# Kernel tuning notes

Measured on AMD Instinct MI355X. Metric: run time of the kernel, lower is better.

Reference implementation:

```python
import jax, jax.numpy as jnp
import numpy as np

K = 16  # neighbors per node (dgl.knn_graph k)


def _knn_indices(centers, k):
    # pairwise squared distances [N, N]
    sq = jnp.sum(centers * centers, axis=1)
    d2 = sq[:, None] + sq[None, :] - 2.0 * (centers @ centers.T)
    # k nearest (includes self at distance ~0), edges: neighbor(src) -> node(dst)
    _, idx = jax.lax.top_k(-d2, k)  # [N, k]
    return idx


def _graph_conv(h, idx, src_norm, dst_norm, W, b):
    # DGL GraphConv, norm='both': D_out^{-1/2} A D_in^{-1/2} H W + b
    hs = h * src_norm[:, None]          # scale by out-degree^{-1/2}
    agg = jnp.sum(hs[idx], axis=1)      # sum over k neighbors -> [N, F]
    agg = agg * dst_norm                # in-degree is exactly k for knn graph
    return agg @ W + b


def setup_inputs() -> dict:
    key = jax.random.key(0)
    ks = jax.random.split(key, 8)
    N, D, H = 20000, 128, 256
    s_in, s_h = 1.0 / np.sqrt(D), 1.0 / np.sqrt(H)
    return {
        "x": jax.random.normal(ks[0], (N, D), dtype=jnp.float32),
        "centers": jax.random.normal(ks[1], (N, 3), dtype=jnp.float32),
        "W0": jax.random.normal(ks[2], (D, H), dtype=jnp.float32) * s_in,
        "b0": jnp.zeros((H,), dtype=jnp.float32),
        "W1": jax.random.normal(ks[3], (H, H), dtype=jnp.float32) * s_h,
        "b1": jnp.zeros((H,), dtype=jnp.float32),
        "W2": jax.random.normal(ks[4], (H, H), dtype=jnp.float32) * s_h,
        "b2": jnp.zeros((H,), dtype=jnp.float32),
        "Wf": jax.random.normal(ks[5], (H, 1), dtype=jnp.float32) * s_h,
        "bf": jnp.zeros((1,), dtype=jnp.float32),
    }


def reference(x, centers, W0, b0, W1, b1, W2, b2, Wf, bf):
    N = x.shape[0]
    idx = _knn_indices(centers, K)  # [N, K] src nodes per dst node
    # out-degree of each node = number of times it appears as a neighbor
    out_deg = jnp.zeros((N,), dtype=x.dtype).at[idx.reshape(-1)].add(1.0)
    src_norm = jax.lax.rsqrt(jnp.maximum(out_deg, 1.0))
    dst_norm = 1.0 / jnp.sqrt(jnp.asarray(K, dtype=x.dtype))  # in-degree == K
    h = x
    for W, b in ((W0, b0), (W1, b1), (W2, b2)):
        h = jax.nn.relu(_graph_conv(h, idx, src_norm, dst_norm, W, b))
    logits = (h @ Wf + bf).squeeze(-1)  # [N]
    return jax.nn.sigmoid(logits)
```

## Files before the change

### kernel.cpp

```cpp
#include <hip/hip_runtime.h>
#include <math.h>

#define KNN 16
#define G 32
#define G3 32768
#define MRING 31
#define FLTMAX 3.402823466e+38f

typedef __attribute__((ext_vector_type(8))) short short8x;
typedef __attribute__((ext_vector_type(4))) float f32x4;

__device__ __forceinline__ unsigned short bf16rn(float x) {
  unsigned u = __float_as_uint(x);
  unsigned r = (u + 0x7FFFu + ((u >> 16) & 1u)) >> 16;
  return (unsigned short)r;
}
__device__ __forceinline__ float bf16tof(unsigned short h) {
  return __uint_as_float(((unsigned)h) << 16);
}

__device__ __forceinline__ unsigned fkey(float f) {
  unsigned u = __float_as_uint(f);
  return (u & 0x80000000u) ? ~u : (u | 0x80000000u);
}
__device__ __forceinline__ float funkey(unsigned u) {
  unsigned b = (u & 0x80000000u) ? (u & 0x7FFFFFFFu) : ~u;
  return __uint_as_float(b);
}

__device__ __forceinline__ void cell_of(float x, float y, float z, const float* P,
                                        int& cx, int& cy, int& cz) {
  cx = min(G - 1, max(0, (int)((x - P[0]) * P[3])));
  cy = min(G - 1, max(0, (int)((y - P[1]) * P[4])));
  cz = min(G - 1, max(0, (int)((z - P[2]) * P[5])));
}

__global__ void init_kernel(int* __restrict__ counts, int* __restrict__ cursor,
                            unsigned* __restrict__ bbox) {
  int t = blockIdx.x * blockDim.x + threadIdx.x;
  if (t < G3) counts[t] = 0;
  int u = t - G3;
  if (u >= 0 && u < G3) cursor[u] = 0;
  if (t == 0) {
    for (int k = 0; k < 3; ++k) { bbox[k] = 0xFFFFFFFFu; bbox[3 + k] = 0u; }
  }
}

__global__ void prep_kernel(const float* __restrict__ centers,
                            float4* __restrict__ cpack,
                            int* __restrict__ deg, unsigned* __restrict__ bbox, int n) {
  #pragma clang fp contract(off)
  int i = blockIdx.x * blockDim.x + threadIdx.x;
  if (i < n) {
    float x = centers[3 * i], y = centers[3 * i + 1], z = centers[3 * i + 2];
    float sq = (x * x + y * y) + z * z;
    cpack[i] = make_float4(x, y, z, sq);
    deg[i] = 0;
    atomicMin(&bbox[0], fkey(x));
    atomicMin(&bbox[1], fkey(y));
    atomicMin(&bbox[2], fkey(z));
    atomicMax(&bbox[3], fkey(x));
    atomicMax(&bbox[4], fkey(y));
    atomicMax(&bbox[5], fkey(z));
  }
}

__global__ void params_kernel(const unsigned* __restrict__ bbox, float* __restrict__ P) {
  if (threadIdx.x == 0 && blockIdx.x == 0) {
    float xmin = funkey(bbox[0]), ymin = funkey(bbox[1]), zmin = funkey(bbox[2]);
    float xmax = funkey(bbox[3]), ymax = funkey(bbox[4]), zmax = funkey(bbox[5]);
    float ex = fmaxf(xmax - xmin, 1e-9f);
    float ey = fmaxf(ymax - ymin, 1e-9f);
    float ez = fmaxf(zmax - zmin, 1e-9f);
    P[0] = xmin; P[1] = ymin; P[2] = zmin;
    P[3] = (float)G / ex; P[4] = (float)G / ey; P[5] = (float)G / ez;
    P[6] = ex / (float)G; P[7] = ey / (float)G; P[8] = ez / (float)G;
    P[9] = fminf(P[6], fminf(P[7], P[8]));
  }
}

__global__ void count_kernel(const float4* __restrict__ cpack, const float* __restrict__ P,
                             int* __restrict__ counts, int n) {
  int i = blockIdx.x * blockDim.x + threadIdx.x;
  if (i >= n) return;
  float4 c = cpack[i];
  int cx, cy, cz; cell_of(c.x, c.y, c.z, P, cx, cy, cz);
  atomicAdd(&counts[(cz * G + cy) * G + cx], 1);
}

__global__ __launch_bounds__(1024) void scan_kernel(const int* __restrict__ counts,
                                                    int* __restrict__ starts,
                                                    int2* __restrict__ cellinfo) {
  __shared__ int sh[1024];
  int t = threadIdx.x;
  int base = t * 32;
  int loc[32];
  int cnts[32];
  int s = 0;
  #pragma unroll
  for (int u = 0; u < 32; ++u) {
    cnts[u] = counts[base + u];
    loc[u] = s; s += cnts[u];
  }
  sh[t] = s;
  __syncthreads();
  for (int off = 1; off < 1024; off <<= 1) {
    int v = (t >= off) ? sh[t - off] : 0;
    __syncthreads();
    sh[t] += v;
    __syncthreads();
  }
  int pre = (t == 0) ? 0 : sh[t - 1];
  #pragma unroll
  for (int u = 0; u < 32; ++u) {
    int st = pre + loc[u];
    starts[base + u] = st;
    cellinfo[base + u] = make_int2(st, cnts[u]);
  }
}

__global__ void scatter_kernel(const float4* __restrict__ cpack, const float* __restrict__ P,
                               const int* __restrict__ starts, int* __restrict__ cursor,
                               int* __restrict__ sid, int* __restrict__ inv,
                               float4* __restrict__ spack, int n) {
  int i = blockIdx.x * blockDim.x + threadIdx.x;
  if (i >= n) return;
  float4 c = cpack[i];
  int cx, cy, cz; cell_of(c.x, c.y, c.z, P, cx, cy, cz);
  int cell = (cz * G + cy) * G + cx;
  int slot = starts[cell] + atomicAdd(&cursor[cell], 1);
  sid[slot] = i;
  inv[i] = slot;
  spack[slot] = c;
}

__global__ __launch_bounds__(64) void query_kernel(
    const float4* __restrict__ spack, const int* __restrict__ sid,
    const int* __restrict__ inv, const int2* __restrict__ cellinfo,
    const float* __restrict__ P, int* __restrict__ knn_idx,
    int* __restrict__ deg, int n) {
  #pragma clang fp contract(off)
  __shared__ unsigned long long lsk[KNN][64];
  const int lane = threadIdx.x;
  const int g = blockIdx.x;
  if (g >= n) return;
  const float4 q = spack[g];
  const float xmin = P[0], ymin = P[1], zmin = P[2];
  const float wx = P[6], wy = P[7], wz = P[8], wmin = P[9];
  int cx, cy, cz; cell_of(q.x, q.y, q.z, P, cx, cy, cz);

  int cnt = 0;
  unsigned long long wkey = 0; int wslot = 0;
  unsigned long long minkey = ~0ull; int minslot = 0;

  for (int m = 1; m <= MRING; ++m) {
    if (m >= 2) {
      float b = (float)(m - 1) * wmin;
      float b2 = b * b * 0.999f;
      unsigned long long tk = ((unsigned long long)fkey(b2)) << 32;
      int c = 0;
      for (int t = 0; t < cnt; ++t) c += (lsk[t][lane] < tk) ? 1 : 0;
      #pragma unroll
      for (int off = 1; off < 64; off <<= 1) c += __shfl_xor(c, off);
      if (c >= KNN) break;
    }
    float lw = (cnt == KNN) ? funkey((unsigned)(wkey >> 32)) : FLTMAX;
    #pragma unroll
    for (int off = 1; off < 64; off <<= 1) lw = fminf(lw, __shfl_xor(lw, off));

    const int ncells = (m == 1) ? 27 : (24 * m * m + 2);
    for (int cb = 0; cb < ncells; cb += 64) {
      int f = cb + lane;
      int ccnt = 0, cs0 = 0;
      if (f < ncells) {
        int dx, dy, dz;
        if (m == 1) {
          dz = f / 9 - 1; int rem = f % 9; dy = rem / 3 - 1; dx = rem % 3 - 1;
        } else {
          int side = 2 * m + 1;
          int S1 = side * side;
          if (f < 2 * S1) {
            dz = (f < S1) ? -m : m;
            int i2 = (f < S1) ? f : f - S1;
            dy = i2 / side - m; dx = i2 % side - m;
          } else {
            int r = f - 2 * S1;
            int layer = r / (8 * m);
            int t2 = r - layer * 8 * m;
            dz = layer - (m - 1);
            if (t2 < side) { dy = -m; dx = t2 - m; }
            else if (t2 < 2 * side) { dy = m; dx = (t2 - side) - m; }
            else { int u = t2 - 2 * side; dx = (u & 1) ? m : -m; dy = (u >> 1) - (m - 1); }
          }
        }
        int x = cx + dx, y = cy + dy, z = cz + dz;
        if (x >= 0 && x < G && y >= 0 && y < G && z >= 0 && z < G) {
          int cell = (z * G + y) * G + x;
          int2 ci = cellinfo[cell];
          if (ci.y > 0) {
            float lox = xmin + (float)x * wx;
            float loy = ymin + (float)y * wy;
            float loz = zmin + (float)z * wz;
            float ddx = fmaxf(fmaxf(lox - q.x, q.x - (lox + wx)), 0.f);
            float ddy = fmaxf(fmaxf(loy - q.y, q.y - (loy + wy)), 0.f);
            float ddz = fmaxf(fmaxf(loz - q.z, q.z - (loz + wz)), 0.f);
            float cd2 = ddx * ddx + ddy * ddy + ddz * ddz;
            if (!(cd2 * 0.999f > lw)) { ccnt = ci.y; cs0 = ci.x; }
          }
        }
      }
      int inc = ccnt;
      #pragma unroll
      for (int off = 1; off < 64; off <<= 1) {
        int t = __shfl_up(inc, off);
        if (lane >= off) inc += t;
      }
      int total = __shfl(inc, 63);
      if (total == 0) continue;
      unsigned seg = ((unsigned)(inc - ccnt) << 16) | (unsigned)cs0;
      const int tmax = total - 1;

      int fc = lane;
      int fcc = min(fc, tmax);
      int lo = 0;
      #pragma unroll
      for (int s = 32; s >= 1; s >>= 1) {
        int cand = lo + s;
        unsigned o = __shfl(seg, cand & 63);
        if (cand < 64 && (int)(o >> 16) <= fcc) lo = cand;
      }
      unsigned o2 = __shfl(seg, lo);
      int src = (int)(o2 & 0xFFFFu) + (fcc - (int)(o2 >> 16));
      float4 c4 = spack[src];
      int j = sid[src];
      const int nloop = (total + 63) >> 6;
      for (int it = 0; it < nloop; ++it) {
        int fn = fc + 64;
        int fnc = min(fn, tmax);
        int lo2 = 0;
        #pragma unroll
        for (int s = 32; s >= 1; s >>= 1) {
          int cand = lo2 + s;
          unsigned o = __shfl(seg, cand & 63);
          if (cand < 64 && (int)(o >> 16) <= fnc) lo2 = cand;
        }
        unsigned o3 = __shfl(seg, lo2);
        int srcn = (int)(o3 & 0xFFFFu) + (fnc - (int)(o3 >> 16));
        float4 c4n = spack[srcn];
        int jn = sid[srcn];
        if (fc < total) {
          float dot = fmaf(q.z, c4.z, fmaf(q.y, c4.y, q.x * c4.x));
          float d2 = (q.w + c4.w) - 2.0f * dot;
          unsigned long long key =
              (((unsigned long long)fkey(d2)) << 32) | (unsigned)j;
          if (cnt < KNN) {
            lsk[cnt][lane] = key;
            if (key < minkey) { minkey = key; minslot = cnt; }
            ++cnt;
            if (cnt == KNN) {
              wkey = 0; wslot = 0;
              #pragma unroll
              for (int u = 0; u < KNN; ++u) {
                unsigned long long k2 = lsk[u][lane];
                if (k2 > wkey) { wkey = k2; wslot = u; }
              }
            }
          } else if (key < wkey) {
            lsk[wslot][lane] = key;
            if (key < minkey) { minkey = key; minslot = wslot; }
            wkey = 0;
            #pragma unroll
            for (int u = 0; u < KNN; ++u) {
              unsigned long long k2 = lsk[u][lane];
              if (k2 > wkey) { wkey = k2; wslot = u; }
            }
          }
        }
        fc = fn; c4 = c4n; j = jn;
      }
    }
  }

  unsigned long long mykey = 0;
  for (int t = 0; t < KNN; ++t) {
    unsigned long long k = minkey; int src = lane;
    #pragma unroll
    for (int off = 1; off < 64; off <<= 1) {
      unsigned long long ok = __shfl_xor(k, off);
      int os = __shfl_xor(src, off);
      if (ok < k) { k = ok; src = os; }
    }
    if (lane == t) mykey = k;
    if (lane == src) {
      lsk[minslot][lane] = ~0ull;
      minkey = ~0ull; minslot = 0;
      for (int u = 0; u < cnt; ++u) {
        unsigned long long kk = lsk[u][lane];
        if (kk < minkey) { minkey = kk; minslot = u; }
      }
    }
  }
  if (lane < KNN) {
    int j = (int)(unsigned)(mykey & 0xFFFFFFFFull);
    int js = inv[j];
    knn_idx[g * KNN + lane] = js;
    atomicAdd(&deg[js], 1);
  }
}

__global__ void norm_kernel(const int* __restrict__ deg, float* __restrict__ srcn, int n) {
  int i = blockIdx.x * blockDim.x + threadIdx.x;
  if (i < n) {
    float d = (float)max(deg[i], 1);
    srcn[i] = 1.0f / sqrtf(d);
  }
}

__global__ void split_w_kernel(const float* __restrict__ W,
                               unsigned short* __restrict__ wbh,
                               unsigned short* __restrict__ wbl, int K) {
  int t = blockIdx.x * blockDim.x + threadIdx.x;
  int noct = (K >> 5) * 1024;
  if (t >= noct) return;
  int kblk = t >> 10;
  int g = (t >> 6) & 15;
  int l = t & 63;
  int n = ((g >> 2) << 6) + ((g & 3) << 4) + (l & 15);
  int kbase = (kblk << 5) + ((l >> 4) << 3);
  #pragma unroll
  for (int j = 0; j < 8; ++j) {
    float w = W[(kbase + j) * 256 + n];
    unsigned short hi = bf16rn(w);
    wbh[t * 8 + j] = hi;
    wbl[t * 8 + j] = bf16rn(w - bf16tof(hi));
  }
}

__device__ __forceinline__ int xcd_swizzle(int b, int grid8) {
  int nch = grid8 >> 3;
  return (b & 7) * nch + (b >> 3);
}

template <int F>
__global__ __launch_bounds__(256) void agg_kernel(const float* __restrict__ h,
                                                  const int* __restrict__ rmap,
                                                  const float* __restrict__ srcn,
                                                  const int* __restrict__ idx,
                                                  unsigned short* __restrict__ ah,
                                                  unsigned short* __restrict__ al,
                                                  int n) {
  const int lane = threadIdx.x & 63;
  const int wv = threadIdx.x >> 6;
  const int eb = xcd_swizzle(blockIdx.x, gridDim.x);
  const int i = eb * 4 + wv;
  if (i >= n) return;
  constexpr int V = F / 64;
  if constexpr (V == 4) {
    float4 acc = make_float4(0.f, 0.f, 0.f, 0.f);
    #pragma unroll
    for (int k = 0; k < KNN; ++k) {
      int s = idx[i * KNN + k];
      float sn = srcn[s];
      int row = rmap ? rmap[s] : s;
      float4 hv = ((const float4*)(h + (size_t)row * F))[lane];
      acc.x = fmaf(sn, hv.x, acc.x);
      acc.y = fmaf(sn, hv.y, acc.y);
      acc.z = fmaf(sn, hv.z, acc.z);
      acc.w = fmaf(sn, hv.w, acc.w);
    }
    acc.x *= 0.25f; acc.y *= 0.25f; acc.z *= 0.25f; acc.w *= 0.25f;
    ushort4 hh, ll;
    hh.x = bf16rn(acc.x); ll.x = bf16rn(acc.x - bf16tof(hh.x));
    hh.y = bf16rn(acc.y); ll.y = bf16rn(acc.y - bf16tof(hh.y));
    hh.z = bf16rn(acc.z); ll.z = bf16rn(acc.z - bf16tof(hh.z));
    hh.w = bf16rn(acc.w); ll.w = bf16rn(acc.w - bf16tof(hh.w));
    ((ushort4*)(ah + (size_t)i * F))[lane] = hh;
    ((ushort4*)(al + (size_t)i * F))[lane] = ll;
  } else {
    float2 acc = make_float2(0.f, 0.f);
    #pragma unroll
    for (int k = 0; k < KNN; ++k) {
      int s = idx[i * KNN + k];
      float sn = srcn[s];
      int row = rmap ? rmap[s] : s;
      float2 hv = ((const float2*)(h + (size_t)row * F))[lane];
      acc.x = fmaf(sn, hv.x, acc.x);
      acc.y = fmaf(sn, hv.y, acc.y);
    }
    acc.x *= 0.25f; acc.y *= 0.25f;
    ushort2 hh, ll;
    hh.x = bf16rn(acc.x); ll.x = bf16rn(acc.x - bf16tof(hh.x));
    hh.y = bf16rn(acc.y); ll.y = bf16rn(acc.y - bf16tof(hh.y));
    ((ushort2*)(ah + (size_t)i * F))[lane] = hh;
    ((ushort2*)(al + (size_t)i * F))[lane] = ll;
  }
}

__global__ __launch_bounds__(256) void gemm_mfma(
    const unsigned short* __restrict__ ah, const unsigned short* __restrict__ al,
    const unsigned short* __restrict__ wbh, const unsigned short* __restrict__ wbl,
    const float* __restrict__ bias, float* __restrict__ C, int M, int Kd) {
  __shared__ unsigned short sa_h[2][64][8];
  __shared__ unsigned short sa_l[2][64][8];
  __shared__ unsigned short sb_h[16][64][8];
  __shared__ unsigned short sb_l[16][64][8];
  const int tid = threadIdx.x;
  const int lane = tid & 63;
  const int w = tid >> 6;
  const int eb = xcd_swizzle(blockIdx.x, gridDim.x);
  const int mt0 = eb * 32;
  if (mt0 >= M) return;

  f32x4 acc[2][4];
  #pragma unroll
  for (int ms = 0; ms < 2; ++ms)
    #pragma unroll
    for (int ns = 0; ns < 4; ++ns) acc[ms][ns] = (f32x4){0.f, 0.f, 0.f, 0.f};

  const int nkb = Kd >> 5;
  for (int kit = 0; kit < nkb; ++kit) {
    const int k0 = kit << 5;
    if (tid < 128) {
      int msub = tid >> 6, l = tid & 63;
      int row = mt0 + (msub << 4) + (l & 15);
      int kk = k0 + ((l >> 4) << 3);
      if (row < M) {
        *(uint4*)&sa_h[msub][l][0] = *(const uint4*)(ah + (size_t)row * Kd + kk);
        *(uint4*)&sa_l[msub][l][0] = *(const uint4*)(al + (size_t)row * Kd + kk);
      } else {
        uint4 z = make_uint4(0, 0, 0, 0);
        *(uint4*)&sa_h[msub][l][0] = z;
        *(uint4*)&sa_l[msub][l][0] = z;
      }
    }
    #pragma unroll
    for (int o = tid; o < 1024; o += 256) {
      size_t off = ((size_t)kit * 1024 + o) * 8;
      *(uint4*)&sb_h[o >> 6][o & 63][0] = *(const uint4*)(wbh + off);
      *(uint4*)&sb_l[o >> 6][o & 63][0] = *(const uint4*)(wbl + off);
    }
    __syncthreads();
    short8x a_h0 = *(const short8x*)&sa_h[0][lane][0];
    short8x a_h1 = *(const short8x*)&sa_h[1][lane][0];
    short8x a_l0 = *(const short8x*)&sa_l[0][lane][0];
    short8x a_l1 = *(const short8x*)&sa_l[1][lane][0];
    #pragma unroll
    for (int ns = 0; ns < 4; ++ns) {
      short8x b_h = *(const short8x*)&sb_h[w * 4 + ns][lane][0];
      short8x b_l = *(const short8x*)&sb_l[w * 4 + ns][lane][0];
      acc[0][ns] = __builtin_amdgcn_mfma_f32_16x16x32_bf16(a_h0, b_h, acc[0][ns], 0, 0, 0);
      acc[0][ns] = __builtin_amdgcn_mfma_f32_16x16x32_bf16(a_h0, b_l, acc[0][ns], 0, 0, 0);
      acc[0][ns] = __builtin_amdgcn_mfma_f32_16x16x32_bf16(a_l0, b_h, acc[0][ns], 0, 0, 0);
      acc[1][ns] = __builtin_amdgcn_mfma_f32_16x16x32_bf16(a_h1, b_h, acc[1][ns], 0, 0, 0);
      acc[1][ns] = __builtin_amdgcn_mfma_f32_16x16x32_bf16(a_h1, b_l, acc[1][ns], 0, 0, 0);
      acc[1][ns] = __builtin_amdgcn_mfma_f32_16x16x32_bf16(a_l1, b_h, acc[1][ns], 0, 0, 0);
    }
    __syncthreads();
  }

  const int col = lane & 15;
  const int rq = lane >> 4;
  #pragma unroll
  for (int ms = 0; ms < 2; ++ms) {
    #pragma unroll
    for (int ns = 0; ns < 4; ++ns) {
      int nn = (w << 6) + (ns << 4) + col;
      float bi = bias[nn];
      #pragma unroll
      for (int r = 0; r < 4; ++r) {
        int row = mt0 + (ms << 4) + (rq << 2) + r;
        if (row < M) C[(size_t)row * 256 + nn] = fmaxf(acc[ms][ns][r] + bi, 0.f);
      }
    }
  }
}

__global__ __launch_bounds__(256) void final_kernel(const float* __restrict__ h,
                                                    const int* __restrict__ sid,
                                                    const float* __restrict__ Wf,
                                                    const float* __restrict__ bf,
                                                    float* __restrict__ out, int n) {
  const int lane = threadIdx.x & 63;
  const int wv = threadIdx.x >> 6;
  const int eb = xcd_swizzle(blockIdx.x, gridDim.x);
  const int i = eb * 4 + wv;
  if (i >= n) return;
  float4 hv = *(const float4*)(h + (size_t)i * 256 + lane * 4);
  float4 wf = *(const float4*)(Wf + lane * 4);
  float p = hv.x * wf.x + hv.y * wf.y + hv.z * wf.z + hv.w * wf.w;
  #pragma unroll
  for (int off = 32; off > 0; off >>= 1) p += __shfl_down(p, off);
  if (lane == 0) out[sid[i]] = 1.0f / (1.0f + expf(-(p + bf[0])));
}

extern "C" void kernel_launch(void* const* d_in, const int* in_sizes, int n_in,
                              void* d_out, int out_size, void* d_ws, size_t ws_size,
                              hipStream_t stream) {
  const float* x = (const float*)d_in[0];
  const float* centers = (const float*)d_in[1];
  const float* W0 = (const float*)d_in[2];
  const float* b0 = (const float*)d_in[3];
  const float* W1 = (const float*)d_in[4];
  const float* b1 = (const float*)d_in[5];
  const float* W2 = (const float*)d_in[6];
  const float* b2 = (const float*)d_in[7];
  const float* Wf = (const float*)d_in[8];
  const float* bf = (const float*)d_in[9];
  float* out = (float*)d_out;

  const int N = in_sizes[1] / 3;

  char* p = (char*)d_ws;
  auto alloc = [&](size_t bytes) {
    void* r = (void*)p;
    p += (bytes + 255) & ~(size_t)255;
    return r;
  };
  float4* cpack = (float4*)alloc((size_t)N * 16);
  int* deg = (int*)alloc((size_t)N * 4);
  float* srcn = (float*)alloc((size_t)N * 4);
  int* idx = (int*)alloc((size_t)N * KNN * 4);
  unsigned short* ahb = (unsigned short*)alloc((size_t)N * 256 * 2);
  unsigned short* alb = (unsigned short*)alloc((size_t)N * 256 * 2);
  float* hA = (float*)alloc((size_t)N * 256 * 4);
  unsigned* bbox = (unsigned*)alloc(6 * 4);
  float* P = (float*)alloc(16 * 4);
  int* counts = (int*)alloc((size_t)G3 * 4);
  int* starts = (int*)alloc((size_t)G3 * 4);
  int* cursor = (int*)alloc((size_t)G3 * 4);
  int2* cellinfo = (int2*)alloc((size_t)G3 * 8);
  int* sid = (int*)alloc((size_t)N * 4);
  int* inv = (int*)alloc((size_t)N * 4);
  float4* spack = (float4*)alloc((size_t)N * 16);
  unsigned short* w0h = (unsigned short*)alloc(128 * 256 * 2);
  unsigned short* w0l = (unsigned short*)alloc(128 * 256 * 2);
  unsigned short* w1h = (unsigned short*)alloc(256 * 256 * 2);
  unsigned short* w1l = (unsigned short*)alloc(256 * 256 * 2);
  unsigned short* w2h = (unsigned short*)alloc(256 * 256 * 2);
  unsigned short* w2l = (unsigned short*)alloc(256 * 256 * 2);
  (void)ws_size; (void)n_in; (void)out_size;

  const int nb = (N + 255) / 256;

  init_kernel<<<256, 256, 0, stream>>>(counts, cursor, bbox);
  prep_kernel<<<nb, 256, 0, stream>>>(centers, cpack, deg, bbox, N);
  split_w_kernel<<<(128 / 32) * 1024 / 256, 256, 0, stream>>>(W0, w0h, w0l, 128);
  split_w_kernel<<<(256 / 32) * 1024 / 256, 256, 0, stream>>>(W1, w1h, w1l, 256);
  split_w_kernel<<<(256 / 32) * 1024 / 256, 256, 0, stream>>>(W2, w2h, w2l, 256);
  params_kernel<<<1, 64, 0, stream>>>(bbox, P);
  count_kernel<<<nb, 256, 0, stream>>>(cpack, P, counts, N);
  scan_kernel<<<1, 1024, 0, stream>>>(counts, starts, cellinfo);
  scatter_kernel<<<nb, 256, 0, stream>>>(cpack, P, starts, cursor, sid, inv, spack, N);
  query_kernel<<<N, 64, 0, stream>>>(spack, sid, inv, cellinfo, P, idx, deg, N);
  norm_kernel<<<nb, 256, 0, stream>>>(deg, srcn, N);

  const int agrid = ((N + 3) / 4 + 7) & ~7;
  const int ggrid = (((N + 31) / 32) + 7) & ~7;

  agg_kernel<128><<<agrid, 256, 0, stream>>>(x, sid, srcn, idx, ahb, alb, N);
  gemm_mfma<<<ggrid, 256, 0, stream>>>(ahb, alb, w0h, w0l, b0, hA, N, 128);

  agg_kernel<256><<<agrid, 256, 0, stream>>>(hA, nullptr, srcn, idx, ahb, alb, N);
  gemm_mfma<<<ggrid, 256, 0, stream>>>(ahb, alb, w1h, w1l, b1, hA, N, 256);

  agg_kernel<256><<<agrid, 256, 0, stream>>>(hA, nullptr, srcn, idx, ahb, alb, N);
  gemm_mfma<<<ggrid, 256, 0, stream>>>(ahb, alb, w2h, w2l, b2, hA, N, 256);

  final_kernel<<<agrid, 256, 0, stream>>>(hA, sid, Wf, bf, out, N);
}
```

Baseline: 478.2 us.

## Fuse init into prep, reduce bbox in block, fuse final projection into last GEMM

Merges the init and prep kernels into one launch and replaces the global atomic bounding-box reduction with a single-block shuffle and shared-memory reduction in params_kernel. In the kNN query it skips the cell-distance pruning math while the current worst distance is still unbounded. The last GEMM now applies ReLU, takes the dot product with Wf, reduces across waves in shared memory and writes the sigmoid output directly, so the final kernel and the write and reread of the last hidden layer disappear. The new prep_kernel uses a fixed 256x256 grid, which silently assumes N is at most 65536, and the single-block bbox scan is serial over N.

New measurement: 447.4 us. 6.4% less time.

```diff
diff --git a/kernel.cpp b/kernel.cpp
--- a/kernel.cpp
+++ b/kernel.cpp
@@ -35,40 +35,57 @@
   cz = min(G - 1, max(0, (int)((z - P[2]) * P[5])));
 }
 
-__global__ void init_kernel(int* __restrict__ counts, int* __restrict__ cursor,
-                            unsigned* __restrict__ bbox) {
+__global__ void prep_kernel(const float* __restrict__ centers,
+                            float4* __restrict__ cpack, int* __restrict__ deg,
+                            int* __restrict__ counts, int* __restrict__ cursor,
+                            int n) {
+  #pragma clang fp contract(off)
   int t = blockIdx.x * blockDim.x + threadIdx.x;
   if (t < G3) counts[t] = 0;
-  int u = t - G3;
-  if (u >= 0 && u < G3) cursor[u] = 0;
-  if (t == 0) {
-    for (int k = 0; k < 3; ++k) { bbox[k] = 0xFFFFFFFFu; bbox[3 + k] = 0u; }
-  }
-}
-
-__global__ void prep_kernel(const float* __restrict__ centers,
-                            float4* __restrict__ cpack,
-                            int* __restrict__ deg, unsigned* __restrict__ bbox, int n) {
-  #pragma clang fp contract(off)
-  int i = blockIdx.x * blockDim.x + threadIdx.x;
-  if (i < n) {
-    float x = centers[3 * i], y = centers[3 * i + 1], z = centers[3 * i + 2];
+  else cursor[t - G3] = 0;
+  if (t < n) {
+    float x = centers[3 * t], y = centers[3 * t + 1], z = centers[3 * t + 2];
     float sq = (x * x + y * y) + z * z;
-    cpack[i] = make_float4(x, y, z, sq);
-    deg[i] = 0;
-    atomicMin(&bbox[0], fkey(x));
-    atomicMin(&bbox[1], fkey(y));
-    atomicMin(&bbox[2], fkey(z));
-    atomicMax(&bbox[3], fkey(x));
-    atomicMax(&bbox[4], fkey(y));
-    atomicMax(&bbox[5], fkey(z));
-  }
-}
-
-__global__ void params_kernel(const unsigned* __restrict__ bbox, float* __restrict__ P) {
-  if (threadIdx.x == 0 && blockIdx.x == 0) {
-    float xmin = funkey(bbox[0]), ymin = funkey(bbox[1]), zmin = funkey(bbox[2]);
-    float xmax = funkey(bbox[3]), ymax = funkey(bbox[4]), zmax = funkey(bbox[5]);
+    cpack[t] = make_float4(x, y, z, sq);
+    deg[t] = 0;
+  }
+}
+
+__global__ __launch_bounds__(1024) void params_kernel(const float4* __restrict__ cpack,
+                                                      float* __restrict__ P, int n) {
+  __shared__ float sminb[16][3], smaxb[16][3];
+  int tid = threadIdx.x;
+  float mnx = FLTMAX, mny = FLTMAX, mnz = FLTMAX;
+  float mxx = -FLTMAX, mxy = -FLTMAX, mxz = -FLTMAX;
+  for (int i = tid; i < n; i += 1024) {
+    float4 c = cpack[i];
+    mnx = fminf(mnx, c.x); mny = fminf(mny, c.y); mnz = fminf(mnz, c.z);
+    mxx = fmaxf(mxx, c.x); mxy = fmaxf(mxy, c.y); mxz = fmaxf(mxz, c.z);
+  }
+  #pragma unroll
+  for (int off = 1; off < 64; off <<= 1) {
+    mnx = fminf(mnx, __shfl_xor(mnx, off));
+    mny = fminf(mny, __shfl_xor(mny, off));
+    mnz = fminf(mnz, __shfl_xor(mnz, off));
+    mxx = fmaxf(mxx, __shfl_xor(mxx, off));
+    mxy = fmaxf(mxy, __shfl_xor(mxy, off));
+    mxz = fmaxf(mxz, __shfl_xor(mxz, off));
+  }
+  if ((tid & 63) == 0) {
+    int w = tid >> 6;
+    sminb[w][0] = mnx; sminb[w][1] = mny; sminb[w][2] = mnz;
+    smaxb[w][0] = mxx; smaxb[w][1] = mxy; smaxb[w][2] = mxz;
+  }
+  __syncthreads();
+  if (tid == 0) {
+    float xmin = sminb[0][0], ymin = sminb[0][1], zmin = sminb[0][2];
+    float xmax = smaxb[0][0], ymax = smaxb[0][1], zmax = smaxb[0][2];
+    for (int w = 1; w < 16; ++w) {
+      xmin = fminf(xmin, sminb[w][0]); ymin = fminf(ymin, sminb[w][1]);
+      zmin = fminf(zmin, sminb[w][2]);
+      xmax = fmaxf(xmax, smaxb[w][0]); ymax = fmaxf(ymax, smaxb[w][1]);
+      zmax = fmaxf(zmax, smaxb[w][2]);
+    }
     float ex = fmaxf(xmax - xmin, 1e-9f);
     float ey = fmaxf(ymax - ymin, 1e-9f);
     float ez = fmaxf(zmax - zmin, 1e-9f);
@@ -167,6 +184,7 @@
     float lw = (cnt == KNN) ? funkey((unsigned)(wkey >> 32)) : FLTMAX;
     #pragma unroll
     for (int off = 1; off < 64; off <<= 1) lw = fminf(lw, __shfl_xor(lw, off));
+    const bool do_prune = (lw < FLTMAX);
 
     const int ncells = (m == 1) ? 27 : (24 * m * m + 2);
     for (int cb = 0; cb < ncells; cb += 64) {
@@ -198,14 +216,18 @@
           int cell = (z * G + y) * G + x;
           int2 ci = cellinfo[cell];
           if (ci.y > 0) {
-            float lox = xmin + (float)x * wx;
-            float loy = ymin + (float)y * wy;
-            float loz = zmin + (float)z * wz;
-            float ddx = fmaxf(fmaxf(lox - q.x, q.x - (lox + wx)), 0.f);
-            float ddy = fmaxf(fmaxf(loy - q.y, q.y - (loy + wy)), 0.f);
-            float ddz = fmaxf(fmaxf(loz - q.z, q.z - (loz + wz)), 0.f);
-            float cd2 = ddx * ddx + ddy * ddy + ddz * ddz;
-            if (!(cd2 * 0.999f > lw)) { ccnt = ci.y; cs0 = ci.x; }
+            bool pass = true;
+            if (do_prune) {
+              float lox = xmin + (float)x * wx;
+              float loy = ymin + (float)y * wy;
+              float loz = zmin + (float)z * wz;
+              float ddx = fmaxf(fmaxf(lox - q.x, q.x - (lox + wx)), 0.f);
+              float ddy = fmaxf(fmaxf(loy - q.y, q.y - (loy + wy)), 0.f);
+              float ddz = fmaxf(fmaxf(loz - q.z, q.z - (loz + wz)), 0.f);
+              float cd2 = ddx * ddx + ddy * ddy + ddz * ddz;
+              pass = !(cd2 * 0.999f > lw);
+            }
+            if (pass) { ccnt = ci.y; cs0 = ci.x; }
           }
         }
       }
@@ -399,11 +421,14 @@
 __global__ __launch_bounds__(256) void gemm_mfma(
     const unsigned short* __restrict__ ah, const unsigned short* __restrict__ al,
     const unsigned short* __restrict__ wbh, const unsigned short* __restrict__ wbl,
-    const float* __restrict__ bias, float* __restrict__ C, int M, int Kd) {
+    const float* __restrict__ bias, float* __restrict__ C, int M, int Kd,
+    const float* __restrict__ Wf, const float* __restrict__ bfp,
+    const int* __restrict__ sid, float* __restrict__ outp) {
   __shared__ unsigned short sa_h[2][64][8];
   __shared__ unsigned short sa_l[2][64][8];
   __shared__ unsigned short sb_h[16][64][8];
   __shared__ unsigned short sb_l[16][64][8];
+  __shared__ float fred[64][4];
   const int tid = threadIdx.x;
   const int lane = tid & 63;
   const int w = tid >> 6;
@@ -460,37 +485,58 @@
 
   const int col = lane & 15;
   const int rq = lane >> 4;
-  #pragma unroll
-  for (int ms = 0; ms < 2; ++ms) {
+  if (Wf) {
+    float pr[2][4];
+    #pragma unroll
+    for (int ms = 0; ms < 2; ++ms)
+      #pragma unroll
+      for (int r = 0; r < 4; ++r) pr[ms][r] = 0.f;
     #pragma unroll
     for (int ns = 0; ns < 4; ++ns) {
       int nn = (w << 6) + (ns << 4) + col;
       float bi = bias[nn];
-      #pragma unroll
-      for (int r = 0; r < 4; ++r) {
-        int row = mt0 + (ms << 4) + (rq << 2) + r;
-        if (row < M) C[(size_t)row * 256 + nn] = fmaxf(acc[ms][ns][r] + bi, 0.f);
-      }
-    }
-  }
-}
-
-__global__ __launch_bounds__(256) void final_kernel(const float* __restrict__ h,
-                                                    const int* __restrict__ sid,
-                                                    const float* __restrict__ Wf,
-                                                    const float* __restrict__ bf,
-                                                    float* __restrict__ out, int n) {
-  const int lane = threadIdx.x & 63;
-  const int wv = threadIdx.x >> 6;
-  const int eb = xcd_swizzle(blockIdx.x, gridDim.x);
-  const int i = eb * 4 + wv;
-  if (i >= n) return;
-  float4 hv = *(const float4*)(h + (size_t)i * 256 + lane * 4);
-  float4 wf = *(const float4*)(Wf + lane * 4);
-  float p = hv.x * wf.x + hv.y * wf.y + hv.z * wf.z + hv.w * wf.w;
-  #pragma unroll
-  for (int off = 32; off > 0; off >>= 1) p += __shfl_down(p, off);
-  if (lane == 0) out[sid[i]] = 1.0f / (1.0f + expf(-(p + bf[0])));
+      float wv = Wf[nn];
+      #pragma unroll
+      for (int ms = 0; ms < 2; ++ms)
+        #pragma unroll
+        for (int r = 0; r < 4; ++r)
+          pr[ms][r] = fmaf(fmaxf(acc[ms][ns][r] + bi, 0.f), wv, pr[ms][r]);
+    }
+    #pragma unroll
+    for (int mask = 1; mask < 16; mask <<= 1)
+      #pragma unroll
+      for (int ms = 0; ms < 2; ++ms)
+        #pragma unroll
+        for (int r = 0; r < 4; ++r) pr[ms][r] += __shfl_xor(pr[ms][r], mask);
+    if (col == 0) {
+      #pragma unroll
+      for (int ms = 0; ms < 2; ++ms)
+        #pragma unroll
+        for (int r = 0; r < 4; ++r) fred[(ms << 4) + (rq << 2) + r][w] = pr[ms][r];
+    }
+    __syncthreads();
+    if (tid < 32) {
+      int row = mt0 + tid;
+      if (row < M) {
+        float s = ((fred[tid][0] + fred[tid][1]) + (fred[tid][2] + fred[tid][3])) + bfp[0];
+        outp[sid[row]] = 1.0f / (1.0f + expf(-s));
+      }
+    }
+  } else {
+    #pragma unroll
+    for (int ms = 0; ms < 2; ++ms) {
+      #pragma unroll
+      for (int ns = 0; ns < 4; ++ns) {
+        int nn = (w << 6) + (ns << 4) + col;
+        float bi = bias[nn];
+        #pragma unroll
+        for (int r = 0; r < 4; ++r) {
+          int row = mt0 + (ms << 4) + (rq << 2) + r;
+          if (row < M) C[(size_t)row * 256 + nn] = fmaxf(acc[ms][ns][r] + bi, 0.f);
+        }
+      }
+    }
+  }
 }
 
 extern "C" void kernel_launch(void* const* d_in, const int* in_sizes, int n_in,
@@ -523,7 +569,6 @@
   unsigned short* ahb = (unsigned short*)alloc((size_t)N * 256 * 2);
   unsigned short* alb = (unsigned short*)alloc((size_t)N * 256 * 2);
   float* hA = (float*)alloc((size_t)N * 256 * 4);
-  unsigned* bbox = (unsigned*)alloc(6 * 4);
   float* P = (float*)alloc(16 * 4);
   int* counts = (int*)alloc((size_t)G3 * 4);
   int* starts = (int*)alloc((size_t)G3 * 4);
@@ -542,12 +587,11 @@
 
   const int nb = (N + 255) / 256;
 
-  init_kernel<<<256, 256, 0, stream>>>(counts, cursor, bbox);
-  prep_kernel<<<nb, 256, 0, stream>>>(centers, cpack, deg, bbox, N);
+  prep_kernel<<<256, 256, 0, stream>>>(centers, cpack, deg, counts, cursor, N);
   split_w_kernel<<<(128 / 32) * 1024 / 256, 256, 0, stream>>>(W0, w0h, w0l, 128);
   split_w_kernel<<<(256 / 32) * 1024 / 256, 256, 0, stream>>>(W1, w1h, w1l, 256);
   split_w_kernel<<<(256 / 32) * 1024 / 256, 256, 0, stream>>>(W2, w2h, w2l, 256);
-  params_kernel<<<1, 64, 0, stream>>>(bbox, P);
+  params_kernel<<<1, 1024, 0, stream>>>(cpack, P, N);
   count_kernel<<<nb, 256, 0, stream>>>(cpack, P, counts, N);
   scan_kernel<<<1, 1024, 0, stream>>>(counts, starts, cellinfo);
   scatter_kernel<<<nb, 256, 0, stream>>>(cpack, P, starts, cursor, sid, inv, spack, N);
@@ -558,13 +602,14 @@
   const int ggrid = (((N + 31) / 32) + 7) & ~7;
 
   agg_kernel<128><<<agrid, 256, 0, stream>>>(x, sid, srcn, idx, ahb, alb, N);
-  gemm_mfma<<<ggrid, 256, 0, stream>>>(ahb, alb, w0h, w0l, b0, hA, N, 128);
+  gemm_mfma<<<ggrid, 256, 0, stream>>>(ahb, alb, w0h, w0l, b0, hA, N, 128,
+                                       nullptr, nullptr, nullptr, nullptr);
 
   agg_kernel<256><<<agrid, 256, 0, stream>>>(hA, nullptr, srcn, idx, ahb, alb, N);
-  gemm_mfma<<<ggrid, 256, 0, stream>>>(ahb, alb, w1h, w1l, b1, hA, N, 256);
+  gemm_mfma<<<ggrid, 256, 0, stream>>>(ahb, alb, w1h, w1l, b1, hA, N, 256,
+                                       nullptr, nullptr, nullptr, nullptr);
 
   agg_kernel<256><<<agrid, 256, 0, stream>>>(hA, nullptr, srcn, idx, ahb, alb, N);
-  gemm_mfma<<<ggrid, 256, 0, stream>>>(ahb, alb, w2h, w2l, b2, hA, N, 256);
-
-  final_kernel<<<agrid, 256, 0, stream>>>(hA, sid, Wf, bf, out, N);
-}
+  gemm_mfma<<<ggrid, 256, 0, stream>>>(ahb, alb, w2h, w2l, b2, nullptr, N, 256,
+                                       Wf, bf, sid, out);
+}
```
